# Kernel optimization log

Measured on AMD Instinct MI355X. Metric: run time of the kernel, lower is better.

The kernel has to match this reference:

```python
import jax, jax.numpy as jnp
import numpy as np

B, C, T = 64, 80, 16384
EPS = 1e-6
QS = (0.25, 0.5, 0.75)


def setup_inputs() -> dict:
    key = jax.random.key(0)
    k1, k2 = jax.random.split(key)
    x = jax.random.normal(k1, (B, C, T), dtype=jnp.float32)
    lengths = jax.random.randint(k2, (B,), T // 2, T + 1, dtype=jnp.int32)
    return {"x": x, "lengths": lengths}


def _stat_pool(x, lengths):
    # x: (B, C, T), lengths: (B,)
    t = jnp.arange(x.shape[-1])
    valid = t[None, :] < lengths[:, None]          # (B, T) bool
    mask = valid[:, None, :].astype(x.dtype)       # (B, 1, T)
    denom = jnp.clip(mask.sum(axis=2), EPS)        # (B, 1)
    mean = (x * mask).sum(axis=2) / denom          # (B, C)
    var = (((x - mean[..., None]) ** 2) * mask).sum(axis=2) / denom
    std = jnp.sqrt(jnp.clip(var, EPS))             # (B, C)

    # Quantiles over valid prefix: push pads to +inf, sort once, gather+lerp.
    x_pad = jnp.where(valid[:, None, :], x, jnp.inf)
    xs = jnp.sort(x_pad, axis=2)                   # (B, C, T), valid values first
    n1 = (lengths - 1).astype(x.dtype)             # (B,) = n-1

    def quantile(q):
        pos = q * n1                               # (B,) fractional index
        lo = jnp.floor(pos).astype(jnp.int32)
        hi = jnp.ceil(pos).astype(jnp.int32)
        w = (pos - lo.astype(x.dtype))[:, None]    # (B, 1)
        xlo = jnp.take_along_axis(xs, lo[:, None, None], axis=2)[..., 0]  # (B, C)
        xhi = jnp.take_along_axis(xs, hi[:, None, None], axis=2)[..., 0]
        return xlo + w * (xhi - xlo)               # torch.quantile 'linear'

    q25, q50, q75 = (quantile(q) for q in QS)
    return jnp.concatenate([mean, std, q25, q50, q75], axis=1)  # (B, 5*C)


def reference(x, lengths):
    return _stat_pool(x, lengths)
```

## Files before the change

kernel.cpp:

```cpp
#include <hip/hip_runtime.h>
#include <stdint.h>

#define BB 64
#define CC 80
#define TT 16384
#define NB 2048
#define CAP 1024
#define NT 256
#define VPT 16

__device__ __forceinline__ int bucket_of(float v) {
    float bf = fmaf(v, 256.0f, 1024.0f);
    bf = fminf(fmaxf(bf, 0.0f), 2047.0f);
    return (int)bf;
}

extern "C" __global__ __launch_bounds__(NT, 4)
void statpool(const float* __restrict__ x, const int* __restrict__ lengths,
              float* __restrict__ out) {
    const int row = blockIdx.x;
    const int b   = row / CC;
    const int c   = row % CC;
    const float* __restrict__ xr = x + (size_t)row * TT;
    const int L   = lengths[b];
    const int tid = threadIdx.x;
    const int lane = tid & 63;
    const int wid  = tid >> 6;

    __shared__ uint32_t hist[NB];
    __shared__ float    cand[CAP];
    __shared__ uint32_t tsum[NT];
    __shared__ float    wsum[4], wsq[4];
    __shared__ int      rbkt[6], rwr[6];
    __shared__ float    wts[3];
    __shared__ uint32_t ccount;

    for (int i = tid; i < NB; i += NT) hist[i] = 0u;
    __syncthreads();

    const int nfull = L >> 2;
    const float4* x4 = (const float4*)xr;
    float4 v4[VPT];
    #pragma unroll
    for (int i = 0; i < VPT; i++) {
        int idx = tid + i * NT;
        v4[i] = make_float4(0.f, 0.f, 0.f, 0.f);
        if (idx < nfull) v4[i] = x4[idx];
    }
    float tailv = 0.f;
    const bool hasTail = tid < (L & 3);
    if (hasTail) tailv = xr[(L & ~3) + tid];

    float sum = 0.f, sq = 0.f;
    #pragma unroll
    for (int i = 0; i < VPT; i++) {
        int idx = tid + i * NT;
        if (idx < nfull) {
            float4 v = v4[i];
            sum += v.x + v.y + v.z + v.w;
            sq  = fmaf(v.x, v.x, fmaf(v.y, v.y, fmaf(v.z, v.z, fmaf(v.w, v.w, sq))));
            atomicAdd(&hist[bucket_of(v.x)], 1u);
            atomicAdd(&hist[bucket_of(v.y)], 1u);
            atomicAdd(&hist[bucket_of(v.z)], 1u);
            atomicAdd(&hist[bucket_of(v.w)], 1u);
        }
    }
    if (hasTail) {
        sum += tailv; sq = fmaf(tailv, tailv, sq);
        atomicAdd(&hist[bucket_of(tailv)], 1u);
    }
    for (int off = 32; off > 0; off >>= 1) {
        sum += __shfl_down(sum, off);
        sq  += __shfl_down(sq,  off);
    }
    if (lane == 0) { wsum[wid] = sum; wsq[wid] = sq; }
    __syncthreads();

    const int base = tid * (NB / NT);
    {
        uint32_t s = 0;
        #pragma unroll
        for (int i = 0; i < NB / NT; i++) s += hist[base + i];
        tsum[tid] = s;
    }
    __syncthreads();

    if (tid < 64) {
        uint32_t a0 = tsum[4*tid+0], a1 = tsum[4*tid+1],
                 a2 = tsum[4*tid+2], a3 = tsum[4*tid+3];
        uint32_t tot = a0 + a1 + a2 + a3;
        uint32_t inc = tot;
        #pragma unroll
        for (int off = 1; off < 64; off <<= 1) {
            uint32_t t = __shfl_up(inc, off);
            if (tid >= off) inc += t;
        }
        uint32_t ex = inc - tot;
        tsum[4*tid+0] = ex;
        tsum[4*tid+1] = ex + a0;
        tsum[4*tid+2] = ex + a0 + a1;
        tsum[4*tid+3] = ex + a0 + a1 + a2;
    } else if (tid == 64) {
        float fs = wsum[0] + wsum[1] + wsum[2] + wsum[3];
        float fq = wsq[0]  + wsq[1]  + wsq[2]  + wsq[3];
        float denom = (float)L;
        float mean = fs / denom;
        float var  = fq / denom - mean * mean;
        float stdv = sqrtf(fmaxf(var, 1e-6f));
        out[(size_t)b * (5*CC) + 0*CC + c] = mean;
        out[(size_t)b * (5*CC) + 1*CC + c] = stdv;
        ccount = 0u;
    }
    __syncthreads();

    {
        uint32_t run = tsum[tid];
        #pragma unroll
        for (int i = 0; i < NB / NT; i++) { run += hist[base + i]; hist[base + i] = run; }
    }
    __syncthreads();

    if (tid < 6) {
        const float qs3[3] = {0.25f, 0.5f, 0.75f};
        const int qi = tid >> 1;
        float pos = qs3[qi] * (float)(L - 1);
        int r = (tid & 1) ? (int)ceilf(pos) : (int)floorf(pos);
        if ((tid & 1) == 0) wts[qi] = pos - floorf(pos);
        int lo = 0, hi = NB - 1;
        while (lo < hi) {
            int mid = (lo + hi) >> 1;
            if (hist[mid] > (uint32_t)r) hi = mid; else lo = mid + 1;
        }
        rbkt[tid] = lo;
        rwr[tid]  = r - (int)(lo ? hist[lo - 1] : 0u);
    }
    __syncthreads();

    const int b0 = rbkt[0], b1 = rbkt[1], b2 = rbkt[2],
              b3 = rbkt[3], b4 = rbkt[4], b5 = rbkt[5];

    auto gthr = [&](float f) {
        int bk = bucket_of(f);
        bool hit = (bk >= b0 && bk <= b1) || (bk >= b2 && bk <= b3) ||
                   (bk >= b4 && bk <= b5);
        if (hit) {
            uint32_t p = atomicAdd(&ccount, 1u);
            if (p < CAP) cand[p] = f;
        }
    };
    #pragma unroll
    for (int i = 0; i < VPT; i++) {
        int idx = tid + i * NT;
        if (idx < nfull) {
            float4 v = v4[i];
            gthr(v.x); gthr(v.y); gthr(v.z); gthr(v.w);
        }
    }
    if (hasTail) gthr(tailv);
    __syncthreads();

    int m = (int)(ccount < (uint32_t)CAP ? ccount : (uint32_t)CAP);
    int n = 1; while (n < m) n <<= 1;
    for (int i = m + tid; i < n; i += NT) cand[i] = __builtin_inff();
    __syncthreads();

    for (int k = 2; k <= n; k <<= 1) {
        for (int j = k >> 1; j > 0; j >>= 1) {
            for (int i = tid; i < n; i += NT) {
                int ixj = i ^ j;
                if (ixj > i) {
                    float a = cand[i], bv = cand[ixj];
                    bool asc = ((i & k) == 0);
                    if (asc ? (a > bv) : (a < bv)) { cand[i] = bv; cand[ixj] = a; }
                }
            }
            __syncthreads();
        }
    }

    if (tid < 3) {
        const int jl = 2 * tid, jh = 2 * tid + 1;
        int bkl = rbkt[jl];
        int lo = 0, hi = n;
        while (lo < hi) { int mid = (lo + hi) >> 1; if (bucket_of(cand[mid]) < bkl) lo = mid + 1; else hi = mid; }
        float xlo = cand[lo + rwr[jl]];
        int bkh = rbkt[jh];
        lo = 0; hi = n;
        while (lo < hi) { int mid = (lo + hi) >> 1; if (bucket_of(cand[mid]) < bkh) lo = mid + 1; else hi = mid; }
        float xhi = cand[lo + rwr[jh]];
        float val = xlo + wts[tid] * (xhi - xlo);
        out[(size_t)b * (5*CC) + (2 + tid) * CC + c] = val;
    }
}

extern "C" void kernel_launch(void* const* d_in, const int* in_sizes, int n_in,
                              void* d_out, int out_size, void* d_ws, size_t ws_size,
                              hipStream_t stream) {
    (void)in_sizes; (void)n_in; (void)out_size; (void)d_ws; (void)ws_size;
    const float* x       = (const float*)d_in[0];
    const int*   lengths = (const int*)d_in[1];
    float*       out     = (float*)d_out;
    hipLaunchKernelGGL(statpool, dim3(BB * CC), dim3(NT), 0, stream, x, lengths, out);
}
```

Baseline: 448.8 us.

## Replace candidate bitonic sort with rank-counting selection; issue loads before hist init

```diff
diff --git a/kernel.cpp b/kernel.cpp
--- a/kernel.cpp
+++ b/kernel.cpp
@@ -15,7 +15,7 @@
     return (int)bf;
 }
 
-extern "C" __global__ __launch_bounds__(NT, 4)
+extern "C" __global__ __launch_bounds__(NT)
 void statpool(const float* __restrict__ x, const int* __restrict__ lengths,
               float* __restrict__ out) {
     const int row = blockIdx.x;
@@ -28,21 +28,21 @@
     const int wid  = tid >> 6;
 
     __shared__ uint32_t hist[NB];
-    __shared__ float    cand[CAP];
+    __shared__ uint2    candp[CAP];
     __shared__ uint32_t tsum[NT];
     __shared__ float    wsum[4], wsq[4];
     __shared__ int      rbkt[6], rwr[6];
+    __shared__ float    res[6];
     __shared__ float    wts[3];
     __shared__ uint32_t ccount;
-
-    for (int i = tid; i < NB; i += NT) hist[i] = 0u;
-    __syncthreads();
 
     const int nfull = L >> 2;
     const float4* x4 = (const float4*)xr;
     float4 v4[VPT];
     #pragma unroll
-    for (int i = 0; i < VPT; i++) {
+    for (int i = 0; i < 8; i++) v4[i] = x4[tid + i * NT];
+    #pragma unroll
+    for (int i = 8; i < VPT; i++) {
         int idx = tid + i * NT;
         v4[i] = make_float4(0.f, 0.f, 0.f, 0.f);
         if (idx < nfull) v4[i] = x4[idx];
@@ -51,11 +51,15 @@
     const bool hasTail = tid < (L & 3);
     if (hasTail) tailv = xr[(L & ~3) + tid];
 
+    for (int i = tid; i < NB; i += NT) hist[i] = 0u;
+    if (tid == 0) ccount = 0u;
+    __syncthreads();
+
     float sum = 0.f, sq = 0.f;
     #pragma unroll
     for (int i = 0; i < VPT; i++) {
         int idx = tid + i * NT;
-        if (idx < nfull) {
+        if (i < 8 || idx < nfull) {
             float4 v = v4[i];
             sum += v.x + v.y + v.z + v.w;
             sq  = fmaf(v.x, v.x, fmaf(v.y, v.y, fmaf(v.z, v.z, fmaf(v.w, v.w, sq))));
@@ -109,7 +113,6 @@
         float stdv = sqrtf(fmaxf(var, 1e-6f));
         out[(size_t)b * (5*CC) + 0*CC + c] = mean;
         out[(size_t)b * (5*CC) + 1*CC + c] = stdv;
-        ccount = 0u;
     }
     __syncthreads();
 
@@ -138,6 +141,8 @@
 
     const int b0 = rbkt[0], b1 = rbkt[1], b2 = rbkt[2],
               b3 = rbkt[3], b4 = rbkt[4], b5 = rbkt[5];
+    const int t0 = rwr[0], t1 = rwr[1], t2 = rwr[2],
+              t3 = rwr[3], t4 = rwr[4], t5 = rwr[5];
 
     auto gthr = [&](float f) {
         int bk = bucket_of(f);
@@ -145,13 +150,13 @@
                    (bk >= b4 && bk <= b5);
         if (hit) {
             uint32_t p = atomicAdd(&ccount, 1u);
-            if (p < CAP) cand[p] = f;
+            if (p < CAP) candp[p] = make_uint2(__float_as_uint(f), (uint32_t)bk);
         }
     };
     #pragma unroll
     for (int i = 0; i < VPT; i++) {
         int idx = tid + i * NT;
-        if (idx < nfull) {
+        if (i < 8 || idx < nfull) {
             float4 v = v4[i];
             gthr(v.x); gthr(v.y); gthr(v.z); gthr(v.w);
         }
@@ -159,37 +164,31 @@
     if (hasTail) gthr(tailv);
     __syncthreads();
 
-    int m = (int)(ccount < (uint32_t)CAP ? ccount : (uint32_t)CAP);
-    int n = 1; while (n < m) n <<= 1;
-    for (int i = m + tid; i < n; i += NT) cand[i] = __builtin_inff();
-    __syncthreads();
-
-    for (int k = 2; k <= n; k <<= 1) {
-        for (int j = k >> 1; j > 0; j >>= 1) {
-            for (int i = tid; i < n; i += NT) {
-                int ixj = i ^ j;
-                if (ixj > i) {
-                    float a = cand[i], bv = cand[ixj];
-                    bool asc = ((i & k) == 0);
-                    if (asc ? (a > bv) : (a < bv)) { cand[i] = bv; cand[ixj] = a; }
-                }
-            }
-            __syncthreads();
-        }
-    }
+    const int m = (int)(ccount < (uint32_t)CAP ? ccount : (uint32_t)CAP);
+    for (int i = tid; i < m; i += NT) {
+        uint2 ci = candp[i];
+        float vi = __uint_as_float(ci.x);
+        int   bi = (int)ci.y;
+        int cnt = 0;
+        for (int j = 0; j < m; j++) {
+            uint2 cj = candp[j];
+            float vj = __uint_as_float(cj.x);
+            bool before = ((int)cj.y == bi) &&
+                          (vj < vi || (vj == vi && j < i));
+            cnt += before ? 1 : 0;
+        }
+        if (bi == b0 && cnt == t0) res[0] = vi;
+        if (bi == b1 && cnt == t1) res[1] = vi;
+        if (bi == b2 && cnt == t2) res[2] = vi;
+        if (bi == b3 && cnt == t3) res[3] = vi;
+        if (bi == b4 && cnt == t4) res[4] = vi;
+        if (bi == b5 && cnt == t5) res[5] = vi;
+    }
+    __syncthreads();
 
     if (tid < 3) {
-        const int jl = 2 * tid, jh = 2 * tid + 1;
-        int bkl = rbkt[jl];
-        int lo = 0, hi = n;
-        while (lo < hi) { int mid = (lo + hi) >> 1; if (bucket_of(cand[mid]) < bkl) lo = mid + 1; else hi = mid; }
-        float xlo = cand[lo + rwr[jl]];
-        int bkh = rbkt[jh];
-        lo = 0; hi = n;
-        while (lo < hi) { int mid = (lo + hi) >> 1; if (bucket_of(cand[mid]) < bkh) lo = mid + 1; else hi = mid; }
-        float xhi = cand[lo + rwr[jh]];
-        float val = xlo + wts[tid] * (xhi - xlo);
-        out[(size_t)b * (5*CC) + (2 + tid) * CC + c] = val;
+        float xlo = res[2*tid], xhi = res[2*tid+1];
+        out[(size_t)b * (5*CC) + (2 + tid) * CC + c] = xlo + wts[tid] * (xhi - xlo);
     }
 }
 
```

New measurement: 486.5 us. 1.08x slower.
